# Kernel optimization log

Hardware: AMD Instinct MI355X
Metric: run time of the kernel (lower is better)

The kernel has to match this reference:

```python
import jax, jax.numpy as jnp
import numpy as np

B, NINP, NMAX, C = 32, 16, 128, 128

def conv1x1(x, w, b):
    # x: [B, cin, n, n], w: [cout, cin], b: [cout]
    return jnp.einsum('bchw,oc->bohw', x, w) + b[None, :, None, None]

def block(x, Msum, wa, ba, wb, bb, wc, bc):
    x1 = jax.nn.relu(conv1x1(x, wa, ba) * Msum)
    x2 = jax.nn.relu(conv1x1(x, wb, bb) * Msum)
    x1x2 = jnp.matmul(x1, x2) * Msum          # batched [B,C,n,n] @ [B,C,n,n]
    return jax.nn.relu(conv1x1(jnp.concatenate([x1x2, x], axis=1), wc, bc) * Msum)

def setup_inputs() -> dict:
    key = jax.random.key(0)
    ks = jax.random.split(key, 32)
    def w(k, o, i, s=0.05):
        return jax.random.normal(k, (o, i), dtype=jnp.float32) * s
    inp = {
        'X2': jax.random.normal(ks[0], (B, NINP, NMAX, NMAX), dtype=jnp.float32),
        'M':  jax.random.uniform(ks[1], (B, 2, NMAX, NMAX), dtype=jnp.float32),
        'w11': w(ks[2], C, NINP), 'b11': jnp.zeros((C,), jnp.float32),
        'w12': w(ks[3], C, NINP), 'b12': jnp.zeros((C,), jnp.float32),
        'w13': w(ks[4], C, C + NINP), 'b13': jnp.zeros((C,), jnp.float32),
        'w21': w(ks[5], C, C), 'b21': jnp.zeros((C,), jnp.float32),
        'w22': w(ks[6], C, C), 'b22': jnp.zeros((C,), jnp.float32),
        'w23': w(ks[7], C, 2 * C), 'b23': jnp.zeros((C,), jnp.float32),
        'w31': w(ks[8], C, C), 'b31': jnp.zeros((C,), jnp.float32),
        'w32': w(ks[9], C, C), 'b32': jnp.zeros((C,), jnp.float32),
        'w33': w(ks[10], C, 2 * C), 'b33': jnp.zeros((C,), jnp.float32),
        'h1w': w(ks[11], 32, 3 * C), 'h1b': jnp.zeros((32,), jnp.float32),
        'h2w': w(ks[12], 1, 32), 'h2b': jnp.zeros((1,), jnp.float32),
    }
    return inp

def reference(X2, M, w11, b11, w12, b12, w13, b13, w21, b21, w22, b22, w23, b23,
              w31, b31, w32, b32, w33, b33, h1w, h1b, h2w, h2b):
    Msum = jnp.sum(M, axis=1, keepdims=True)   # [B,1,n,n]
    Mdiag = M[:, 0:1]                          # [B,1,n,n]
    x = X2
    x = block(x, Msum, w11, b11, w12, b12, w13, b13)
    xo1 = jnp.sum(x * Mdiag, axis=(2, 3))      # [B,C]
    x = block(x, Msum, w21, b21, w22, b22, w23, b23)
    xo2 = jnp.sum(x * Mdiag, axis=(2, 3))
    x = block(x, Msum, w31, b31, w32, b32, w33, b33)
    xo3 = jnp.sum(x * Mdiag, axis=(2, 3))
    h = jnp.concatenate([xo1, xo2, xo3], axis=1)
    h = jax.nn.relu(h @ h1w.T + h1b)
    return h @ h2w.T + h2b                     # [B,1]
```

## Files before the change

### kernel.cpp

```cpp
#include <hip/hip_runtime.h>
#include <stdint.h>
#include <stddef.h>

#define NBATCH 32
#define HW     16384
#define CCH    128
#define WROW   40
#define WCHUNK 10240

typedef short bf16x8 __attribute__((ext_vector_type(8)));
typedef float f32x4  __attribute__((ext_vector_type(4)));

__device__ __forceinline__ float bf2f(unsigned short u){
    union { unsigned int i; float f; } v; v.i = ((unsigned int)u) << 16; return v.f;
}
__device__ __forceinline__ unsigned short f2bf(float f){
    union { float f; unsigned int i; } v; v.f = f;
    unsigned int x = v.i;
    x += 0x7fffu + ((x >> 16) & 1u);
    return (unsigned short)(x >> 16);
}
__device__ __forceinline__ unsigned int h16(uint2 u, int j){
    unsigned int v = (j & 2) ? u.y : u.x;
    return (j & 1) ? (v >> 16) : (v & 0xffffu);
}
__device__ __forceinline__ void gl_lds16(const unsigned short* g, unsigned short* l){
    __builtin_amdgcn_global_load_lds(
        reinterpret_cast<const __attribute__((address_space(1))) unsigned int*>(
            reinterpret_cast<uintptr_t>(g)),
        reinterpret_cast<__attribute__((address_space(3))) unsigned int*>(
            reinterpret_cast<uintptr_t>(l)),
        16, 0, 0);
}
template<int N> __device__ __forceinline__ void vmwait(){
    asm volatile("s_waitcnt vmcnt(%0)" :: "n"(N) : "memory");
}

#define WPREP_TOTAL 399360
__global__ __launch_bounds__(256) void k_setup(
    const float* __restrict__ w11, const float* __restrict__ w12, const float* __restrict__ w13,
    const float* __restrict__ w21, const float* __restrict__ w22, const float* __restrict__ w23,
    const float* __restrict__ w31, const float* __restrict__ w32, const float* __restrict__ w33,
    const float* __restrict__ M,
    unsigned short* __restrict__ wp, float* __restrict__ msum, float* __restrict__ xo)
{
    int i = blockIdx.x*256 + threadIdx.x;
    {
        int b = i >> 14, hw = i & (HW-1);
        msum[i] = M[(size_t)b*2*HW + hw] + M[(size_t)b*2*HW + HW + hw];
    }
    if(i < NBATCH*384) xo[i] = 0.f;
    if(i < WPREP_TOTAL){
        const float* src; int K, mode, base;
        if     (i < 10240) { src=w11; K=16;  mode=1; base=0;      }
        else if(i < 20480) { src=w12; K=16;  mode=1; base=10240;  }
        else if(i < 71680) { src=w13; K=144; mode=2; base=20480;  }
        else if(i < 112640){ src=w21; K=128; mode=0; base=71680;  }
        else if(i < 153600){ src=w22; K=128; mode=0; base=112640; }
        else if(i < 235520){ src=w23; K=256; mode=0; base=153600; }
        else if(i < 276480){ src=w31; K=128; mode=0; base=235520; }
        else if(i < 317440){ src=w32; K=128; mode=0; base=276480; }
        else               { src=w33; K=256; mode=0; base=317440; }
        int j  = i - base;
        int ck = j / WCHUNK;
        int jj = j - ck*WCHUNK;
        int half = jj / 5120;
        int rr   = (jj / WROW) & 127;
        int c    = jj % WROW;
        float v = 0.f;
        if(c < 32){
            int col = (mode==1) ? (c & 15)
                    : (mode==2) ? (ck < 4 ? ck*32 + c : 128 + (c & 15))
                    :             ck*32 + c;
            v = src[rr*K + col];
        }
        unsigned short hi = f2bf(v);
        wp[i] = half ? f2bf(v - bf2f(hi)) : hi;
    }
}

template<int NCHP, int NCHX, bool CC, bool XS, bool STORE>
__global__ __launch_bounds__(256,2) void k_conv(
    const unsigned short* __restrict__ Wp,
    const unsigned short* __restrict__ Psrc,
    const void* __restrict__ Xsrc,
    const float* __restrict__ biasA, const float* __restrict__ biasB,
    const float* __restrict__ msum, const float* __restrict__ Mfull,
    unsigned short* __restrict__ OutA, unsigned short* __restrict__ OutB,
    float* __restrict__ xo, int b0, int xo_off)
{
    constexpr int NCH = NCHP + NCHX;
    __shared__ unsigned short Wl[2*WCHUNK];
    __shared__ unsigned short Xt[2*10240];
    const int bi = blockIdx.y, bg = b0 + bi;
    const int hw0 = blockIdx.x * 256;
    const int z = CC ? 0 : blockIdx.z;
    const int t = threadIdx.x;
    const int w = t >> 6, l = t & 63;
    const int lr = l & 15, lg = l >> 4;
    const int wm = w & 1, wn = w >> 1;
    const int cg = t & 3, h4 = t >> 2;
    const unsigned short* Wseg  = Wp + (size_t)z*NCH*WCHUNK;
    const unsigned short* pbase = Psrc + (size_t)bi*CCH*HW;
    const float* xfbase = nullptr;
    const unsigned short* xbbase = nullptr;
    if constexpr (XS) xfbase = (const float*)Xsrc + (size_t)bg*16*HW;
    else              xbbase = (const unsigned short*)Xsrc + (size_t)bi*CCH*HW;

    f32x4 acc[4][8];
    #pragma unroll
    for(int mf=0; mf<4; mf++)
        #pragma unroll
        for(int nf=0; nf<8; nf++) acc[mf][nf] = (f32x4){0.f,0.f,0.f,0.f};

    uint2 xr0[8], xr1[8];
    float xf0[16], xf1[16];

    auto wdma = [&](int ck){
        const unsigned short* s = Wseg + (size_t)ck*WCHUNK + (size_t)t*8;
        unsigned short* d = &Wl[(ck & 1)*WCHUNK + t*8];
        #pragma unroll
        for(int r=0; r<5; r++)
            gl_lds16(s + (size_t)r*2048, d + r*2048);
    };
    auto loadXb = [&](int ck, uint2 (&xr)[8]){
        const unsigned short* s = ((ck < NCHP) ? (pbase + (size_t)ck*32*HW)
                                               : (xbbase + (size_t)(ck-NCHP)*32*HW))
                                  + hw0 + h4*4;
        #pragma unroll
        for(int i=0;i<8;i++) xr[i] = *reinterpret_cast<const uint2*>(s + (size_t)(cg*8+i)*HW);
    };
    auto loadXf = [&](float (&xf)[16]){
        const float* s = xfbase + hw0 + t;
        #pragma unroll
        for(int c=0;c<16;c++) xf[c] = s[(size_t)c*HW];
    };
    auto writeXb = [&](int buf, uint2 (&xr)[8]){
        #pragma unroll
        for(int j=0;j<4;j++){
            uint4 pk;
            pk.x = h16(xr[0],j) | (h16(xr[1],j) << 16);
            pk.y = h16(xr[2],j) | (h16(xr[3],j) << 16);
            pk.z = h16(xr[4],j) | (h16(xr[5],j) << 16);
            pk.w = h16(xr[6],j) | (h16(xr[7],j) << 16);
            *reinterpret_cast<uint4*>(&Xt[buf*10240 + (h4*4+j)*WROW + cg*8]) = pk;
        }
    };
    auto writeXf = [&](int buf, float (&xf)[16]){
        unsigned int hi[16], lo[16];
        #pragma unroll
        for(int c=0;c<16;c++){
            unsigned short h = f2bf(xf[c]);
            hi[c] = h;
            lo[c] = f2bf(xf[c] - bf2f(h));
        }
        uint4 a, b2, c4, d;
        a.x  = hi[0] |(hi[1] <<16); a.y  = hi[2] |(hi[3] <<16); a.z  = hi[4] |(hi[5] <<16); a.w  = hi[6] |(hi[7] <<16);
        b2.x = hi[8] |(hi[9] <<16); b2.y = hi[10]|(hi[11]<<16); b2.z = hi[12]|(hi[13]<<16); b2.w = hi[14]|(hi[15]<<16);
        c4.x = lo[0] |(lo[1] <<16); c4.y = lo[2] |(lo[3] <<16); c4.z = lo[4] |(lo[5] <<16); c4.w = lo[6] |(lo[7] <<16);
        d.x  = lo[8] |(lo[9] <<16); d.y  = lo[10]|(lo[11]<<16); d.z  = lo[12]|(lo[13]<<16); d.w  = lo[14]|(lo[15]<<16);
        unsigned short* base = &Xt[buf*10240 + t*WROW];
        *reinterpret_cast<uint4*>(base +  0) = a;
        *reinterpret_cast<uint4*>(base +  8) = b2;
        *reinterpret_cast<uint4*>(base + 16) = c4;
        *reinterpret_cast<uint4*>(base + 24) = d;
    };
    auto compute = [&](int buf){
        const unsigned short* Wb = &Wl[buf*WCHUNK];
        const unsigned short* Xb = &Xt[buf*10240];
        bf16x8 ah[4], al[4];
        #pragma unroll
        for(int mf=0; mf<4; mf++){
            ah[mf] = *reinterpret_cast<const bf16x8*>(&Wb[(wm*64 + mf*16 + lr)*WROW + lg*8]);
            al[mf] = *reinterpret_cast<const bf16x8*>(&Wb[(128 + wm*64 + mf*16 + lr)*WROW + lg*8]);
        }
        #pragma unroll
        for(int nf=0; nf<8; nf++){
            bf16x8 bfr = *reinterpret_cast<const bf16x8*>(&Xb[(wn*128 + nf*16 + lr)*WROW + lg*8]);
            #pragma unroll
            for(int mf=0; mf<4; mf++){
                acc[mf][nf] = __builtin_amdgcn_mfma_f32_16x16x32_bf16(ah[mf], bfr, acc[mf][nf], 0,0,0);
                acc[mf][nf] = __builtin_amdgcn_mfma_f32_16x16x32_bf16(al[mf], bfr, acc[mf][nf], 0,0,0);
            }
        }
    };

#define LOADC(CK, S) \
    if constexpr ((CK) < NCHP || !XS){ \
        if constexpr ((S)==0) loadXb((CK), xr0); else loadXb((CK), xr1); \
    } else { \
        if constexpr ((S)==0) loadXf(xf0); else loadXf(xf1); \
    }

    LOADC(0, 0)
    __builtin_amdgcn_sched_barrier(0);
    wdma(0);
    __builtin_amdgcn_sched_barrier(0);
    if constexpr (NCH > 1){ LOADC(1, 1) }
    __builtin_amdgcn_sched_barrier(0);

#define STEP(I) \
    if constexpr ((I) < NCH){ \
        vmwait<(((I)+1 < NCH) ? ((((I)+1) < NCHP) ? 8 : (XS ? 16 : 8)) : 0)>(); \
        __builtin_amdgcn_sched_barrier(0); \
        if constexpr ((I) < NCHP || !XS){ \
            if constexpr (((I)&1)==0) writeXb((I)&1, xr0); else writeXb((I)&1, xr1); \
        } else { \
            if constexpr (((I)&1)==0) writeXf((I)&1, xf0); else writeXf((I)&1, xf1); \
        } \
        asm volatile("s_waitcnt lgkmcnt(0)" ::: "memory"); \
        __builtin_amdgcn_sched_barrier(0); \
        __builtin_amdgcn_s_barrier(); \
        if constexpr ((I)+1 < NCH) wdma((I)+1); \
        __builtin_amdgcn_sched_barrier(0); \
        if constexpr ((I)+2 < NCH){ LOADC((I)+2, (I)&1) } \
        __builtin_amdgcn_sched_barrier(0); \
        __builtin_amdgcn_s_setprio(1); \
        compute((I)&1); \
        __builtin_amdgcn_s_setprio(0); \
    }
    STEP(0) STEP(1) STEP(2) STEP(3) STEP(4) STEP(5) STEP(6) STEP(7)
#undef STEP
#undef LOADC

    float msv[8], mdv[8];
    #pragma unroll
    for(int nf=0; nf<8; nf++){
        int hwi = hw0 + wn*128 + nf*16 + lr;
        msv[nf] = msum[(size_t)bg*HW + hwi];
        if constexpr (CC) mdv[nf] = Mfull[(size_t)bg*2*HW + hwi];
    }
    if constexpr (!CC){
        const float* bias = z ? biasB : biasA;
        unsigned short* dst = (z ? OutB : OutA) + (size_t)bi*CCH*HW;
        #pragma unroll
        for(int mf=0; mf<4; mf++){
            #pragma unroll
            for(int reg=0; reg<4; reg++){
                int row = wm*64 + mf*16 + lg*4 + reg;
                float bv = bias[row];
                #pragma unroll
                for(int nf=0; nf<8; nf++){
                    float v2 = (acc[mf][nf][reg] + bv) * msv[nf];
                    v2 = v2 > 0.f ? v2 : 0.f;
                    dst[(size_t)row*HW + hw0 + wn*128 + nf*16 + lr] = f2bf(v2);
                }
            }
        }
    } else {
        unsigned short* dst = OutA + (size_t)bi*CCH*HW;
        #pragma unroll
        for(int mf=0; mf<4; mf++){
            float red[4] = {0.f,0.f,0.f,0.f};
            #pragma unroll
            for(int reg=0; reg<4; reg++){
                int row = wm*64 + mf*16 + lg*4 + reg;
                float bv = biasA[row];
                #pragma unroll
                for(int nf=0; nf<8; nf++){
                    float v2 = (acc[mf][nf][reg] + bv) * msv[nf];
                    v2 = v2 > 0.f ? v2 : 0.f;
                    if constexpr (STORE)
                        dst[(size_t)row*HW + hw0 + wn*128 + nf*16 + lr] = f2bf(v2);
                    red[reg] += v2 * mdv[nf];
                }
            }
            #pragma unroll
            for(int reg=0; reg<4; reg++){
                float r = red[reg];
                r += __shfl_xor(r, 1);
                r += __shfl_xor(r, 2);
                r += __shfl_xor(r, 4);
                r += __shfl_xor(r, 8);
                if(lr == 0)
                    atomicAdd(&xo[(size_t)bg*384 + xo_off + wm*64 + mf*16 + lg*4 + reg], r);
            }
        }
    }
}

__global__ __launch_bounds__(256) void k_bmm(
    const unsigned short* __restrict__ A, const unsigned short* __restrict__ Bm,
    const float* __restrict__ msum, unsigned short* __restrict__ P, int b0)
{
    __shared__ unsigned short Bs[128*136];
    const int m  = blockIdx.x;
    const int bi = m >> 7;
    const int bg = b0 + bi;
    const unsigned short* Ab = A  + (size_t)m*HW;
    const unsigned short* Bb = Bm + (size_t)m*HW;
    unsigned short*       Pb = P  + (size_t)m*HW;
    const float* ms = msum + (size_t)bg*HW;
    const int t = threadIdx.x;
    const int w  = t >> 6;
    const int l  = t & 63;
    const int lr = l & 15;
    const int lg = l >> 4;

    bf16x8 af[4][2];
    #pragma unroll
    for(int kk=0;kk<4;kk++)
        #pragma unroll
        for(int rt=0;rt<2;rt++)
            af[kk][rt] = *reinterpret_cast<const bf16x8*>(Ab + (size_t)(w*32 + rt*16 + lr)*128 + kk*32 + lg*8);

    #pragma unroll
    for(int it=0; it<8; it++){
        int task = it*256 + t;
        int j  = task & 127;
        int kg = task >> 7;
        unsigned short v[8];
        #pragma unroll
        for(int i=0;i<8;i++) v[i] = Bb[(size_t)(kg*8+i)*128 + j];
        uint4 pk;
        pk.x = (unsigned int)v[0] | ((unsigned int)v[1]<<16);
        pk.y = (unsigned int)v[2] | ((unsigned int)v[3]<<16);
        pk.z = (unsigned int)v[4] | ((unsigned int)v[5]<<16);
        pk.w = (unsigned int)v[6] | ((unsigned int)v[7]<<16);
        *reinterpret_cast<uint4*>(&Bs[j*136 + kg*8]) = pk;
    }
    __syncthreads();

    f32x4 acc[2][8];
    #pragma unroll
    for(int rt=0;rt<2;rt++)
        #pragma unroll
        for(int ct=0;ct<8;ct++) acc[rt][ct] = (f32x4){0.f,0.f,0.f,0.f};

    #pragma unroll
    for(int kk=0;kk<4;kk++){
        #pragma unroll
        for(int ct=0;ct<8;ct++){
            bf16x8 bfr = *reinterpret_cast<const bf16x8*>(&Bs[(ct*16+lr)*136 + kk*32 + lg*8]);
            acc[0][ct] = __builtin_amdgcn_mfma_f32_16x16x32_bf16(af[kk][0], bfr, acc[0][ct], 0,0,0);
            acc[1][ct] = __builtin_amdgcn_mfma_f32_16x16x32_bf16(af[kk][1], bfr, acc[1][ct], 0,0,0);
        }
    }
    #pragma unroll
    for(int rt=0;rt<2;rt++){
        #pragma unroll
        for(int ct=0;ct<8;ct++){
            #pragma unroll
            for(int r=0;r<4;r++){
                int row = w*32 + rt*16 + lg*4 + r;
                int col = ct*16 + lr;
                float v = acc[rt][ct][r] * ms[row*128 + col];
                Pb[(size_t)row*128 + col] = f2bf(v);
            }
        }
    }
}

__global__ __launch_bounds__(1024) void k_head(
    const float* __restrict__ xo, const float* __restrict__ h1w, const float* __restrict__ h1b,
    const float* __restrict__ h2w, const float* __restrict__ h2b, float* __restrict__ out)
{
    __shared__ float hbuf[NBATCH][32];
    const int t = threadIdx.x;
    const int b = t >> 5, j = t & 31;
    float a = h1b[j];
    #pragma unroll 8
    for(int k=0;k<384;k++) a += xo[b*384+k]*h1w[j*384+k];
    a = a > 0.f ? a : 0.f;
    hbuf[b][j] = a;
    __syncthreads();
    if(j == 0){
        float s = h2b[0];
        #pragma unroll
        for(int k=0;k<32;k++) s += hbuf[b][k]*h2w[k];
        out[b] = s;
    }
}

extern "C" void kernel_launch(void* const* d_in, const int* in_sizes, int n_in,
                              void* d_out, int out_size, void* d_ws, size_t ws_size,
                              hipStream_t stream)
{
    (void)in_sizes; (void)n_in; (void)out_size;
    const float* X2  = (const float*)d_in[0];
    const float* M   = (const float*)d_in[1];
    const float* w11 = (const float*)d_in[2];  const float* b11 = (const float*)d_in[3];
    const float* w12 = (const float*)d_in[4];  const float* b12 = (const float*)d_in[5];
    const float* w13 = (const float*)d_in[6];  const float* b13 = (const float*)d_in[7];
    const float* w21 = (const float*)d_in[8];  const float* b21 = (const float*)d_in[9];
    const float* w22 = (const float*)d_in[10]; const float* b22 = (const float*)d_in[11];
    const float* w23 = (const float*)d_in[12]; const float* b23 = (const float*)d_in[13];
    const float* w31 = (const float*)d_in[14]; const float* b31 = (const float*)d_in[15];
    const float* w32 = (const float*)d_in[16]; const float* b32 = (const float*)d_in[17];
    const float* w33 = (const float*)d_in[18]; const float* b33 = (const float*)d_in[19];
    const float* h1w = (const float*)d_in[20]; const float* h1b = (const float*)d_in[21];
    const float* h2w = (const float*)d_in[22]; const float* h2b = (const float*)d_in[23];
    float* out = (float*)d_out;

    char* ws = (char*)d_ws;
    size_t off = 0;
    float* msum = (float*)(ws + off); off += (size_t)NBATCH*HW*4;
    float* xo   = (float*)(ws + off); off += (size_t)NBATCH*384*4;
    unsigned short* wp = (unsigned short*)(ws + off); off += (size_t)WPREP_TOTAL*2;
    off = (off + 255) & ~(size_t)255;

    int bc = 32;
    while (bc > 1 && off + 3ull*(size_t)bc*CCH*HW*2 > ws_size) bc >>= 1;
    size_t bufb = (size_t)bc*CCH*HW*2;
    unsigned short* B0 = (unsigned short*)(ws + off);
    unsigned short* B1 = (unsigned short*)(ws + off + bufb);
    unsigned short* B2 = (unsigned short*)(ws + off + 2*bufb);

    const unsigned short* Wa1 = wp + 0;
    const unsigned short* Wc1 = wp + 20480;
    const unsigned short* Wa2 = wp + 71680;
    const unsigned short* Wc2 = wp + 153600;
    const unsigned short* Wa3 = wp + 235520;
    const unsigned short* Wc3 = wp + 317440;

    k_setup<<<(NBATCH*HW)/256, 256, 0, stream>>>(
        w11,w12,w13,w21,w22,w23,w31,w32,w33, M, wp, msum, xo);

    for(int b0 = 0; b0 < NBATCH; b0 += bc){
        dim3 gab(HW/256, bc, 2);
        dim3 gcc(HW/256, bc);
        dim3 gmat(bc*CCH);
        k_conv<0,1,false,true ,true ><<<gab, 256, 0, stream>>>(Wa1, B0, X2, b11, b12, msum, M, B0, B1, nullptr, b0, 0);
        k_bmm<<<gmat, 256, 0, stream>>>(B0, B1, msum, B0, b0);
        k_conv<4,1,true ,true ,true ><<<gcc, 256, 0, stream>>>(Wc1, B0, X2, b13, b13, msum, M, B1, nullptr, xo, b0, 0);
        k_conv<0,4,false,false,true ><<<gab, 256, 0, stream>>>(Wa2, B0, B1, b21, b22, msum, M, B2, B0, nullptr, b0, 0);
        k_bmm<<<gmat, 256, 0, stream>>>(B2, B0, msum, B2, b0);
        k_conv<4,4,true ,false,true ><<<gcc, 256, 0, stream>>>(Wc2, B2, B1, b23, b23, msum, M, B0, nullptr, xo, b0, 128);
        k_conv<0,4,false,false,true ><<<gab, 256, 0, stream>>>(Wa3, B2, B0, b31, b32, msum, M, B1, B2, nullptr, b0, 0);
        k_bmm<<<gmat, 256, 0, stream>>>(B1, B2, msum, B1, b0);
        k_conv<4,4,true ,false,false><<<gcc, 256, 0, stream>>>(Wc3, B1, B0, b33, b33, msum, M, B2, nullptr, xo, b0, 256);
    }
    k_head<<<1, 1024, 0, stream>>>(xo, h1w, h1b, h2w, h2b, out);
}
```

Measured before the change: 1.141 ms.

## Fuse paired A/B 1x1 convs into one 512-thread block sharing staged input

Measured after the change: 1.133 ms. About the same (-0.7%).

```diff
diff --git a/kernel.cpp b/kernel.cpp
--- a/kernel.cpp
+++ b/kernel.cpp
@@ -79,6 +79,167 @@
     }
 }
 
+template<int NCH, bool XS>
+__global__ __launch_bounds__(512,2) void k_cab2(
+    const unsigned short* __restrict__ Wp,
+    const void* __restrict__ Xsrc,
+    const float* __restrict__ biasA, const float* __restrict__ biasB,
+    const float* __restrict__ msum,
+    unsigned short* __restrict__ OutA, unsigned short* __restrict__ OutB, int b0)
+{
+    __shared__ unsigned short Wl[2*2*WCHUNK];
+    __shared__ unsigned short Xt[2*10240];
+    const int bi = blockIdx.y, bg = b0 + bi;
+    const int ht = blockIdx.x;
+    const int hw0 = ht * 256;
+    const int t = threadIdx.x;
+    const int w = t >> 6, l = t & 63;
+    const int lr = l & 15, lg = l >> 4;
+    const int z  = w >> 2;
+    const int wsub = w & 3;
+    const int wm = wsub & 1, wn = wsub >> 1;
+    const int cgx = t & 7, h4x = t >> 3;
+    const float* xfbase = nullptr;
+    const unsigned short* xbbase = nullptr;
+    if constexpr (XS) xfbase = (const float*)Xsrc + (size_t)bg*16*HW;
+    else              xbbase = (const unsigned short*)Xsrc + (size_t)bi*CCH*HW;
+
+    f32x4 acc[4][8];
+    #pragma unroll
+    for(int mf=0; mf<4; mf++)
+        #pragma unroll
+        for(int nf=0; nf<8; nf++) acc[mf][nf] = (f32x4){0.f,0.f,0.f,0.f};
+
+    uint2 xr0[4], xr1[4];
+    float xf0[8], xf1[8];
+
+    auto wdma = [&](int ck){
+        #pragma unroll
+        for(int r=0; r<5; r++){
+            int idx = r*512 + t;
+            int seg = idx / 1280;
+            int off = (idx - seg*1280) * 8;
+            gl_lds16(Wp + (size_t)seg*NCH*WCHUNK + (size_t)ck*WCHUNK + off,
+                     &Wl[(ck & 1)*2*WCHUNK + seg*WCHUNK + off]);
+        }
+    };
+    auto loadXb = [&](int ck, uint2 (&xr)[4]){
+        const unsigned short* s = xbbase + (size_t)ck*32*HW + hw0 + h4x*4;
+        #pragma unroll
+        for(int i=0;i<4;i++) xr[i] = *reinterpret_cast<const uint2*>(s + (size_t)(cgx*4+i)*HW);
+    };
+    auto loadXf = [&](float (&xf)[8]){
+        const int c0 = (t >> 8) * 8;
+        const float* s = xfbase + hw0 + (t & 255);
+        #pragma unroll
+        for(int c=0;c<8;c++) xf[c] = s[(size_t)(c0+c)*HW];
+    };
+    auto writeXb = [&](int buf, uint2 (&xr)[4]){
+        #pragma unroll
+        for(int j=0;j<4;j++){
+            uint2 v;
+            v.x = h16(xr[0],j) | (h16(xr[1],j) << 16);
+            v.y = h16(xr[2],j) | (h16(xr[3],j) << 16);
+            *reinterpret_cast<uint2*>(&Xt[buf*10240 + (h4x*4+j)*WROW + cgx*4]) = v;
+        }
+    };
+    auto writeXf = [&](int buf, float (&xf)[8]){
+        const int c0 = (t >> 8) * 8;
+        const int hwl = t & 255;
+        unsigned int hi[8], lo[8];
+        #pragma unroll
+        for(int c=0;c<8;c++){
+            unsigned short h = f2bf(xf[c]);
+            hi[c] = h;
+            lo[c] = f2bf(xf[c] - bf2f(h));
+        }
+        uint4 a, b2;
+        a.x  = hi[0]|(hi[1]<<16); a.y  = hi[2]|(hi[3]<<16); a.z  = hi[4]|(hi[5]<<16); a.w  = hi[6]|(hi[7]<<16);
+        b2.x = lo[0]|(lo[1]<<16); b2.y = lo[2]|(lo[3]<<16); b2.z = lo[4]|(lo[5]<<16); b2.w = lo[6]|(lo[7]<<16);
+        unsigned short* base = &Xt[buf*10240 + hwl*WROW];
+        *reinterpret_cast<uint4*>(base + c0)      = a;
+        *reinterpret_cast<uint4*>(base + 16 + c0) = b2;
+    };
+    auto compute = [&](int buf){
+        const unsigned short* Wb = &Wl[buf*2*WCHUNK + z*WCHUNK];
+        const unsigned short* Xb = &Xt[buf*10240];
+        bf16x8 ah[4], al[4];
+        #pragma unroll
+        for(int mf=0; mf<4; mf++){
+            ah[mf] = *reinterpret_cast<const bf16x8*>(&Wb[(wm*64 + mf*16 + lr)*WROW + lg*8]);
+            al[mf] = *reinterpret_cast<const bf16x8*>(&Wb[(128 + wm*64 + mf*16 + lr)*WROW + lg*8]);
+        }
+        #pragma unroll
+        for(int nf=0; nf<8; nf++){
+            bf16x8 bfr = *reinterpret_cast<const bf16x8*>(&Xb[(wn*128 + nf*16 + lr)*WROW + lg*8]);
+            #pragma unroll
+            for(int mf=0; mf<4; mf++){
+                acc[mf][nf] = __builtin_amdgcn_mfma_f32_16x16x32_bf16(ah[mf], bfr, acc[mf][nf], 0,0,0);
+                acc[mf][nf] = __builtin_amdgcn_mfma_f32_16x16x32_bf16(al[mf], bfr, acc[mf][nf], 0,0,0);
+            }
+        }
+    };
+
+#define LOADC2(CK, S) \
+    if constexpr (XS){ \
+        if constexpr ((S)==0) loadXf(xf0); else loadXf(xf1); \
+    } else { \
+        if constexpr ((S)==0) loadXb((CK), xr0); else loadXb((CK), xr1); \
+    }
+
+    LOADC2(0, 0)
+    __builtin_amdgcn_sched_barrier(0);
+    wdma(0);
+    __builtin_amdgcn_sched_barrier(0);
+    if constexpr (NCH > 1){ LOADC2(1, 1) }
+    __builtin_amdgcn_sched_barrier(0);
+
+#define STEP(I) \
+    if constexpr ((I) < NCH){ \
+        vmwait<(((I)+1 < NCH) ? (XS ? 8 : 4) : 0)>(); \
+        __builtin_amdgcn_sched_barrier(0); \
+        if constexpr (XS){ \
+            if constexpr (((I)&1)==0) writeXf((I)&1, xf0); else writeXf((I)&1, xf1); \
+        } else { \
+            if constexpr (((I)&1)==0) writeXb((I)&1, xr0); else writeXb((I)&1, xr1); \
+        } \
+        asm volatile("s_waitcnt lgkmcnt(0)" ::: "memory"); \
+        __builtin_amdgcn_sched_barrier(0); \
+        __builtin_amdgcn_s_barrier(); \
+        if constexpr ((I)+1 < NCH) wdma((I)+1); \
+        __builtin_amdgcn_sched_barrier(0); \
+        if constexpr ((I)+2 < NCH){ LOADC2((I)+2, (I)&1) } \
+        __builtin_amdgcn_sched_barrier(0); \
+        __builtin_amdgcn_s_setprio(1); \
+        compute((I)&1); \
+        __builtin_amdgcn_s_setprio(0); \
+    }
+    STEP(0) STEP(1) STEP(2) STEP(3)
+#undef STEP
+#undef LOADC2
+
+    float msv[8];
+    #pragma unroll
+    for(int nf=0; nf<8; nf++)
+        msv[nf] = msum[(size_t)bg*HW + hw0 + wn*128 + nf*16 + lr];
+    const float* bias = z ? biasB : biasA;
+    unsigned short* dst = (z ? OutB : OutA) + (size_t)bi*CCH*HW;
+    #pragma unroll
+    for(int mf=0; mf<4; mf++){
+        #pragma unroll
+        for(int reg=0; reg<4; reg++){
+            int row = wm*64 + mf*16 + lg*4 + reg;
+            float bv = bias[row];
+            #pragma unroll
+            for(int nf=0; nf<8; nf++){
+                float v2 = (acc[mf][nf][reg] + bv) * msv[nf];
+                v2 = v2 > 0.f ? v2 : 0.f;
+                dst[(size_t)row*HW + hw0 + wn*128 + nf*16 + lr] = f2bf(v2);
+            }
+        }
+    }
+}
+
 template<int NCHP, int NCHX, bool CC, bool XS, bool STORE>
 __global__ __launch_bounds__(256,2) void k_conv(
     const unsigned short* __restrict__ Wp,
@@ -94,7 +255,7 @@
     __shared__ unsigned short Xt[2*10240];
     const int bi = blockIdx.y, bg = b0 + bi;
     const int hw0 = blockIdx.x * 256;
-    const int z = CC ? 0 : blockIdx.z;
+    const int z = 0;
     const int t = threadIdx.x;
     const int w = t >> 6, l = t & 63;
     const int lr = l & 15, lg = l >> 4;
@@ -231,8 +392,8 @@
         if constexpr (CC) mdv[nf] = Mfull[(size_t)bg*2*HW + hwi];
     }
     if constexpr (!CC){
-        const float* bias = z ? biasB : biasA;
-        unsigned short* dst = (z ? OutB : OutA) + (size_t)bi*CCH*HW;
+        const float* bias = biasA;
+        unsigned short* dst = OutA + (size_t)bi*CCH*HW;
         #pragma unroll
         for(int mf=0; mf<4; mf++){
             #pragma unroll
@@ -247,6 +408,7 @@
                 }
             }
         }
+        (void)biasB; (void)OutB;
     } else {
         unsigned short* dst = OutA + (size_t)bi*CCH*HW;
         #pragma unroll
@@ -417,16 +579,16 @@
         w11,w12,w13,w21,w22,w23,w31,w32,w33, M, wp, msum, xo);
 
     for(int b0 = 0; b0 < NBATCH; b0 += bc){
-        dim3 gab(HW/256, bc, 2);
+        dim3 gab(64, bc);
         dim3 gcc(HW/256, bc);
         dim3 gmat(bc*CCH);
-        k_conv<0,1,false,true ,true ><<<gab, 256, 0, stream>>>(Wa1, B0, X2, b11, b12, msum, M, B0, B1, nullptr, b0, 0);
+        k_cab2<1,true ><<<gab, 512, 0, stream>>>(Wa1, X2, b11, b12, msum, B0, B1, b0);
         k_bmm<<<gmat, 256, 0, stream>>>(B0, B1, msum, B0, b0);
         k_conv<4,1,true ,true ,true ><<<gcc, 256, 0, stream>>>(Wc1, B0, X2, b13, b13, msum, M, B1, nullptr, xo, b0, 0);
-        k_conv<0,4,false,false,true ><<<gab, 256, 0, stream>>>(Wa2, B0, B1, b21, b22, msum, M, B2, B0, nullptr, b0, 0);
+        k_cab2<4,false><<<gab, 512, 0, stream>>>(Wa2, B1, b21, b22, msum, B2, B0, b0);
         k_bmm<<<gmat, 256, 0, stream>>>(B2, B0, msum, B2, b0);
         k_conv<4,4,true ,false,true ><<<gcc, 256, 0, stream>>>(Wc2, B2, B1, b23, b23, msum, M, B0, nullptr, xo, b0, 128);
-        k_conv<0,4,false,false,true ><<<gab, 256, 0, stream>>>(Wa3, B2, B0, b31, b32, msum, M, B1, B2, nullptr, b0, 0);
+        k_cab2<4,false><<<gab, 512, 0, stream>>>(Wa3, B0, b31, b32, msum, B1, B2, b0);
         k_bmm<<<gmat, 256, 0, stream>>>(B1, B2, msum, B1, b0);
         k_conv<4,4,true ,false,false><<<gcc, 256, 0, stream>>>(Wc3, B1, B0, b33, b33, msum, M, B2, nullptr, xo, b0, 256);
     }
```
